# Kernel optimization log

Measured on AMD Instinct MI355X. Metric: run time of the kernel, lower is better.

## Reference

```python
import jax, jax.numpy as jnp
import numpy as np

BATCH, SEQ, DIMS, HEADS = 4, 2048, 1024, 16
HEAD_DIM = DIMS // HEADS          # 64
ROT = HEAD_DIM // 2               # 32
BASE = 10000.0


def setup_inputs() -> dict:
    key = jax.random.key(0)
    k1, k2, k3, k4 = jax.random.split(key, 4)
    x = jax.random.normal(k1, (BATCH, SEQ, DIMS), jnp.float32)
    thetas = jax.random.normal(k2, (ROT,), jnp.float32) * 0.02
    theta_scale = jnp.ones((1,), jnp.float32)
    # nn.init.orthogonal_ equivalent
    a = jax.random.normal(k3, (HEAD_DIM, HEAD_DIM), jnp.float32)
    r_matrix, _ = jnp.linalg.qr(a)
    inv_freq = 1.0 / (BASE ** (jnp.arange(0, HEAD_DIM, 2, dtype=jnp.float32) / HEAD_DIM))
    # r_pairs: torch rand(rot,2)*head_dim then .long() -> ints in [0, head_dim)
    pairs = jax.random.randint(k4, (ROT, 2), 0, HEAD_DIM, dtype=jnp.int32)
    return {"x": x, "thetas": thetas, "theta_scale": theta_scale,
            "r_matrix": r_matrix, "inv_freq": inv_freq, "pairs": pairs}


def _forward(x, thetas, theta_scale, r_matrix, inv_freq, pairs):
    B, S, D = x.shape
    hd = r_matrix.shape[0]
    H = D // hd
    ts = theta_scale[0]
    xf = x.reshape(-1, hd)  # (B*S*H, hd)

    # Sequential Givens rotations: x @ G_k, applied as 2-column updates.
    # G[i,i]=c, G[j,j]=c, G[i,j]=-s, G[j,i]=s. If i==j, sequential torch
    def body(xx, k):
        i, j = pairs[k, 0], pairs[k, 1]
        th = thetas[k] * ts
        c, s = jnp.cos(th), jnp.sin(th)
        xi = xx[:, i]
        xj = xx[:, j]
        ni = xi * c + xj * s
        nj = jnp.where(i == j, xi * s, xj * c - xi * s)
        xx = xx.at[:, i].set(ni)
        xx = xx.at[:, j].set(nj)  # overwrites column i when i == j
        return xx, None

    xf, _ = jax.lax.scan(body, xf, jnp.arange(pairs.shape[0]))
    xf = xf @ r_matrix
    xh = xf.reshape(B, S, H, hd)

    # rotary sin/cos encoding (concatenated halves, not interleaved)
    pos = jnp.arange(S, dtype=x.dtype)[:, None]          # (S, 1)
    si = pos * inv_freq[None, :]                          # (S, hd//2)
    sin = jnp.sin(si)[None, :, None, :]                   # (1, S, 1, hd//2)
    cos = jnp.cos(si)[None, :, None, :]
    x1, x2 = xh[..., ::2], xh[..., 1::2]
    out = jnp.concatenate([x1 * cos - x2 * sin, x1 * sin + x2 * cos], axis=-1)
    return out.reshape(B, S, D) * jnp.sqrt(jnp.asarray(D, x.dtype))


def reference(x, thetas, theta_scale, r_matrix, inv_freq, pairs):
    return _forward(x, thetas, theta_scale, r_matrix, inv_freq, pairs)
```

## Files before the change

kernel.cpp:

```cpp
#include <hip/hip_runtime.h>
#include <math.h>

#define SEQ    2048
#define ROT    32
#define ROWS_PER_BLOCK 128
#define NTILES (131072 / ROWS_PER_BLOCK)

#define AS1 __attribute__((address_space(1)))
#define AS3 __attribute__((address_space(3)))

__global__ __launch_bounds__(256) void build_w_kernel(
    const float* __restrict__ thetas,
    const float* __restrict__ theta_scale,
    const float* __restrict__ R,
    const int*   __restrict__ pairs,
    float*       __restrict__ W)
{
    __shared__ float A[64 * 65];
    __shared__ float Rs[64 * 64];
    __shared__ float Cs[ROT], Ss[ROT];
    __shared__ int   Pi[ROT], Pj[ROT];
    const int t    = threadIdx.x;
    const int wave = t >> 6;
    const int lane = t & 63;

    #pragma unroll
    for (int i = 0; i < 16; ++i) {
        int e = i * 256 + t;
        int r = e >> 6, c = e & 63;
        A[r * 65 + c] = (r == c) ? 1.0f : 0.0f;
    }
    if (t < ROT) {
        float th = thetas[t] * theta_scale[0];
        float sv, cv;
        sincosf(th, &sv, &cv);
        Cs[t] = cv; Ss[t] = sv;
        Pi[t] = pairs[2 * t]; Pj[t] = pairs[2 * t + 1];
    }
    __syncthreads();

    #pragma unroll
    for (int i = 0; i < 4; ++i) {
        int ri  = i * 4 + wave;
        int row = ri * 4 + (lane >> 4);
        const float* gp = R + row * 64 + (lane & 15) * 4;
        __builtin_amdgcn_global_load_lds((const AS1 unsigned int*)gp,
                                         (AS3 unsigned int*)&Rs[ri * 256], 16, 0, 0);
    }

    if (t < 64) {
        float* Ar = &A[t * 65];
        for (int k = 0; k < ROT; ++k) {
            int i = Pi[k], j = Pj[k];
            float c = Cs[k], s = Ss[k];
            float ai = Ar[i], aj = Ar[j];
            if (i != j) { Ar[i] = c * ai + s * aj; Ar[j] = c * aj - s * ai; }
            else        { Ar[i] = s * ai; }
        }
    }
    __syncthreads();

    const int r = (blockIdx.x << 2) + (t >> 6);
    const int c = t & 63;
    const float* Ar = &A[r * 65];
    float acc = 0.0f;
    #pragma unroll 8
    for (int k = 0; k < 64; ++k)
        acc = fmaf(Ar[k], Rs[k * 64 + c], acc);
    W[r * 64 + c] = 32.0f * acc;
}

__global__ __launch_bounds__(256) void rotary_main_kernel(
    const float* __restrict__ x,
    const float* __restrict__ W,
    const float* __restrict__ inv_freq,
    float*       __restrict__ out)
{
    __shared__ float Ws[64 * 64];
    __shared__ float SCc[8 * 32];
    __shared__ float SCs[8 * 32];

    const int T    = blockIdx.x;
    const int t    = threadIdx.x;
    const int wave = t >> 6;
    const int lane = t & 63;

    #pragma unroll
    for (int i = 0; i < 4; ++i) {
        int ri  = i * 4 + wave;
        int row = ri * 4 + (lane >> 4);
        const float* gp = W + row * 64 + (lane & 15) * 4;
        __builtin_amdgcn_global_load_lds((const AS1 unsigned int*)gp,
                                         (AS3 unsigned int*)&Ws[ri * 256], 16, 0, 0);
    }
    {
        int pg = t >> 5, d = t & 31;
        int pos = (T * 8 + pg) & (SEQ - 1);
        float sv, cv;
        sincosf((float)pos * inv_freq[d], &sv, &cv);
        SCc[t] = cv;
        SCs[t] = sv;
    }

    const int rp = t >> 3;
    const int cg = t & 7;
    const int r0 = rp * 4;
    const float* xr0 = x + (size_t)T * (ROWS_PER_BLOCK * 64) + r0 * 64;
    float4 nx[4];
    #pragma unroll
    for (int m = 0; m < 4; ++m)
        nx[m] = *(const float4*)(xr0 + m * 64);

    __syncthreads();

    float acc[4][8];
    #pragma unroll
    for (int m = 0; m < 4; ++m)
        #pragma unroll
        for (int j = 0; j < 8; ++j) acc[m][j] = 0.0f;

    #pragma unroll 4
    for (int kk = 0; kk < 16; ++kk) {
        float4 xv[4];
        #pragma unroll
        for (int m = 0; m < 4; ++m) xv[m] = nx[m];
        if (kk < 15) {
            #pragma unroll
            for (int m = 0; m < 4; ++m)
                nx[m] = *(const float4*)(xr0 + m * 64 + ((kk + 1) << 2));
        }
        float4 wv[8];
        #pragma unroll
        for (int r = 0; r < 4; ++r) {
            wv[2 * r]     = *(const float4*)&Ws[(4 * kk + r) * 64 + cg * 8];
            wv[2 * r + 1] = *(const float4*)&Ws[(4 * kk + r) * 64 + cg * 8 + 4];
        }
        #pragma unroll
        for (int m = 0; m < 4; ++m) {
            const float xa[4] = {xv[m].x, xv[m].y, xv[m].z, xv[m].w};
            #pragma unroll
            for (int r = 0; r < 4; ++r) {
                const float4 w0 = wv[2 * r], w1 = wv[2 * r + 1];
                const float xs = xa[r];
                acc[m][0] = fmaf(xs, w0.x, acc[m][0]);
                acc[m][1] = fmaf(xs, w0.y, acc[m][1]);
                acc[m][2] = fmaf(xs, w0.z, acc[m][2]);
                acc[m][3] = fmaf(xs, w0.w, acc[m][3]);
                acc[m][4] = fmaf(xs, w1.x, acc[m][4]);
                acc[m][5] = fmaf(xs, w1.y, acc[m][5]);
                acc[m][6] = fmaf(xs, w1.z, acc[m][6]);
                acc[m][7] = fmaf(xs, w1.w, acc[m][7]);
            }
        }
    }

    const int scb = ((r0 >> 4) << 5) + cg * 4;
    const float4 cv = *(const float4*)&SCc[scb];
    const float4 sv = *(const float4*)&SCs[scb];
    const float cs4[4] = {cv.x, cv.y, cv.z, cv.w};
    const float sn4[4] = {sv.x, sv.y, sv.z, sv.w};

    float* og = out + (size_t)T * (ROWS_PER_BLOCK * 64);
    #pragma unroll
    for (int m = 0; m < 4; ++m) {
        int row = r0 + m;
        float o1[4], o2[4];
        #pragma unroll
        for (int d = 0; d < 4; ++d) {
            float a = acc[m][2 * d];
            float b = acc[m][2 * d + 1];
            o1[d] = a * cs4[d] - b * sn4[d];
            o2[d] = a * sn4[d] + b * cs4[d];
        }
        *(float4*)&og[row * 64 + cg * 4]      = make_float4(o1[0], o1[1], o1[2], o1[3]);
        *(float4*)&og[row * 64 + 32 + cg * 4] = make_float4(o2[0], o2[1], o2[2], o2[3]);
    }
}

extern "C" void kernel_launch(void* const* d_in, const int* in_sizes, int n_in,
                              void* d_out, int out_size, void* d_ws, size_t ws_size,
                              hipStream_t stream) {
    const float* x           = (const float*)d_in[0];
    const float* thetas      = (const float*)d_in[1];
    const float* theta_scale = (const float*)d_in[2];
    const float* r_matrix    = (const float*)d_in[3];
    const float* inv_freq    = (const float*)d_in[4];
    const int*   pairs       = (const int*)d_in[5];
    float*       out         = (float*)d_out;
    float*       W           = (float*)d_ws;

    build_w_kernel<<<16, 256, 0, stream>>>(thetas, theta_scale, r_matrix, pairs, W);
    rotary_main_kernel<<<NTILES, 256, 0, stream>>>(x, W, inv_freq, out);
}
```

Before: 106.3 us.

## Fuse W-matrix construction into main kernel by applying Givens rotations to R rows

Removes the separate build_w kernel and its global workspace round-trip. Each block now loads R into shared memory and applies the Givens rotations in reverse order to R's rows, which yields G·R. The scale factor sqrt(D) is folded into the sin/cos tables. This drops one kernel launch and the dependency between the two kernels. In exchange every block redoes a serial 32-step rotation pass over 64 columns plus an extra barrier before the matmul.

```diff
diff --git a/kernel.cpp b/kernel.cpp
--- a/kernel.cpp
+++ b/kernel.cpp
@@ -9,76 +9,20 @@
 #define AS1 __attribute__((address_space(1)))
 #define AS3 __attribute__((address_space(3)))
 
-__global__ __launch_bounds__(256) void build_w_kernel(
+__global__ __launch_bounds__(256) void rotary_fused_kernel(
+    const float* __restrict__ x,
     const float* __restrict__ thetas,
     const float* __restrict__ theta_scale,
     const float* __restrict__ R,
+    const float* __restrict__ inv_freq,
     const int*   __restrict__ pairs,
-    float*       __restrict__ W)
-{
-    __shared__ float A[64 * 65];
-    __shared__ float Rs[64 * 64];
-    __shared__ float Cs[ROT], Ss[ROT];
-    __shared__ int   Pi[ROT], Pj[ROT];
-    const int t    = threadIdx.x;
-    const int wave = t >> 6;
-    const int lane = t & 63;
-
-    #pragma unroll
-    for (int i = 0; i < 16; ++i) {
-        int e = i * 256 + t;
-        int r = e >> 6, c = e & 63;
-        A[r * 65 + c] = (r == c) ? 1.0f : 0.0f;
-    }
-    if (t < ROT) {
-        float th = thetas[t] * theta_scale[0];
-        float sv, cv;
-        sincosf(th, &sv, &cv);
-        Cs[t] = cv; Ss[t] = sv;
-        Pi[t] = pairs[2 * t]; Pj[t] = pairs[2 * t + 1];
-    }
-    __syncthreads();
-
-    #pragma unroll
-    for (int i = 0; i < 4; ++i) {
-        int ri  = i * 4 + wave;
-        int row = ri * 4 + (lane >> 4);
-        const float* gp = R + row * 64 + (lane & 15) * 4;
-        __builtin_amdgcn_global_load_lds((const AS1 unsigned int*)gp,
-                                         (AS3 unsigned int*)&Rs[ri * 256], 16, 0, 0);
-    }
-
-    if (t < 64) {
-        float* Ar = &A[t * 65];
-        for (int k = 0; k < ROT; ++k) {
-            int i = Pi[k], j = Pj[k];
-            float c = Cs[k], s = Ss[k];
-            float ai = Ar[i], aj = Ar[j];
-            if (i != j) { Ar[i] = c * ai + s * aj; Ar[j] = c * aj - s * ai; }
-            else        { Ar[i] = s * ai; }
-        }
-    }
-    __syncthreads();
-
-    const int r = (blockIdx.x << 2) + (t >> 6);
-    const int c = t & 63;
-    const float* Ar = &A[r * 65];
-    float acc = 0.0f;
-    #pragma unroll 8
-    for (int k = 0; k < 64; ++k)
-        acc = fmaf(Ar[k], Rs[k * 64 + c], acc);
-    W[r * 64 + c] = 32.0f * acc;
-}
-
-__global__ __launch_bounds__(256) void rotary_main_kernel(
-    const float* __restrict__ x,
-    const float* __restrict__ W,
-    const float* __restrict__ inv_freq,
     float*       __restrict__ out)
 {
     __shared__ float Ws[64 * 64];
     __shared__ float SCc[8 * 32];
     __shared__ float SCs[8 * 32];
+    __shared__ float Cs[ROT], Ss[ROT];
+    __shared__ int   Pi[ROT], Pj[ROT];
 
     const int T    = blockIdx.x;
     const int t    = threadIdx.x;
@@ -89,17 +33,26 @@
     for (int i = 0; i < 4; ++i) {
         int ri  = i * 4 + wave;
         int row = ri * 4 + (lane >> 4);
-        const float* gp = W + row * 64 + (lane & 15) * 4;
+        const float* gp = R + row * 64 + (lane & 15) * 4;
         __builtin_amdgcn_global_load_lds((const AS1 unsigned int*)gp,
                                          (AS3 unsigned int*)&Ws[ri * 256], 16, 0, 0);
     }
+
+    if (t < ROT) {
+        float th = thetas[t] * theta_scale[0];
+        float sv, cv;
+        sincosf(th, &sv, &cv);
+        Cs[t] = cv; Ss[t] = sv;
+        Pi[t] = pairs[2 * t]; Pj[t] = pairs[2 * t + 1];
+    }
+
     {
         int pg = t >> 5, d = t & 31;
         int pos = (T * 8 + pg) & (SEQ - 1);
         float sv, cv;
         sincosf((float)pos * inv_freq[d], &sv, &cv);
-        SCc[t] = cv;
-        SCs[t] = sv;
+        SCc[t] = 32.0f * cv;
+        SCs[t] = 32.0f * sv;
     }
 
     const int rp = t >> 3;
@@ -111,6 +64,22 @@
     for (int m = 0; m < 4; ++m)
         nx[m] = *(const float4*)(xr0 + m * 64);
 
+    __syncthreads();
+
+    if (t < 64) {
+        for (int k = ROT - 1; k >= 0; --k) {
+            int i = Pi[k], j = Pj[k];
+            float c = Cs[k], s = Ss[k];
+            float wi = Ws[i * 64 + t];
+            if (i != j) {
+                float wj = Ws[j * 64 + t];
+                Ws[i * 64 + t] = c * wi - s * wj;
+                Ws[j * 64 + t] = s * wi + c * wj;
+            } else {
+                Ws[i * 64 + t] = s * wi;
+            }
+        }
+    }
     __syncthreads();
 
     float acc[4][8];
@@ -187,8 +156,8 @@
     const float* inv_freq    = (const float*)d_in[4];
     const int*   pairs       = (const int*)d_in[5];
     float*       out         = (float*)d_out;
-    float*       W           = (float*)d_ws;
+    (void)d_ws; (void)ws_size;
 
-    build_w_kernel<<<16, 256, 0, stream>>>(thetas, theta_scale, r_matrix, pairs, W);
-    rotary_main_kernel<<<NTILES, 256, 0, stream>>>(x, W, inv_freq, out);
+    rotary_fused_kernel<<<NTILES, 256, 0, stream>>>(
+        x, thetas, theta_scale, r_matrix, inv_freq, pairs, out);
 }
```

Measured after the change: 106.8 us. About the same (+0.5%).
